# Kernel optimization log

Measured on AMD Instinct MI355X. Metric: run time of the kernel, lower is better.

## Reference

```python
import jax, jax.numpy as jnp
import numpy as np

P = 4  # polynomial kernel degree


def setup_inputs() -> dict:
    key = jax.random.key(0)
    k1, k2, k3, k4 = jax.random.split(key, 4)
    m, n, d = 16384, 8192, 64
    x_p = jax.random.normal(k1, (m, d), dtype=jnp.float32)
    X = jax.random.normal(k2, (n, d), dtype=jnp.float32)
    alpha = jax.random.uniform(k3, (n,), dtype=jnp.float32, minval=0.0, maxval=0.2)
    b = jax.random.uniform(k4, (1,), dtype=jnp.float32, minval=0.0, maxval=0.2)
    return {"x_p": x_p, "X": X, "alpha": alpha, "b": b}


def reference(x_p, X, alpha, b):
    # SVR prediction with polynomial kernel, vectorized:
    # f(x_p) = sum_i alpha_i * (1 + x_p . X_i)^P + b
    # x_p: [m, d], X: [n, d] -> K: [m, n]
    K = (1.0 + jnp.einsum('md,nd->mn', x_p, X)) ** P
    return K @ alpha + b  # [m]
```

## Files before the change

### kernel.cpp

```cpp
#include <hip/hip_runtime.h>
#include <hip/hip_bf16.h>
#include <stdint.h>


typedef __attribute__((ext_vector_type(8))) short bf16x8;
typedef __attribute__((ext_vector_type(8))) unsigned short ushort8;
typedef __attribute__((ext_vector_type(4))) float f32x4;

#define MM 16384
#define NN 8192
#define DD 64
#define NSPLIT 4
#define CHUNK 64
#define CHUNKS_PER_BLK 32
#define BM 128

__device__ __forceinline__ unsigned short f2bf(float f) {
    uint32_t u = __float_as_uint(f);
    uint32_t r = (u + 0x7FFFu + ((u >> 16) & 1u)) >> 16;
    return (unsigned short)r;
}

__device__ __forceinline__ void gll16(const void* g, void* l) {
    __builtin_amdgcn_global_load_lds(
        (const __attribute__((address_space(1))) unsigned int*)g,
        (__attribute__((address_space(3))) unsigned int*)l, 16, 0, 0);
}

__global__ void convert_kernel(const float* __restrict__ xp,
                               const float* __restrict__ X,
                               const float* __restrict__ alpha,
                               unsigned short* __restrict__ xbf,
                               unsigned short* __restrict__ Xs,
                               float* __restrict__ alpha4f) {
    const int xp4 = MM * DD / 4;
    const int xu = NN * DD / 8;
    const int tot = xp4 + xu;
    int tid0 = blockIdx.x * blockDim.x + threadIdx.x;
    if (tid0 < NN) alpha4f[tid0] = sqrtf(sqrtf(alpha[tid0]));
    int stride = gridDim.x * blockDim.x;
    for (int i = tid0; i < tot; i += stride) {
        if (i < xp4) {
            float4 v = ((const float4*)xp)[i];
            ushort4 o;
            o.x = f2bf(v.x); o.y = f2bf(v.y); o.z = f2bf(v.z); o.w = f2bf(v.w);
            *(ushort4*)(xbf + (size_t)i * 4) = o;
        } else {
            int u = i - xp4;
            int n = u >> 3;
            int slot = u & 7;
            float a4 = sqrtf(sqrtf(alpha[n]));
            float4 va = ((const float4*)X)[n * 16 + slot * 2];
            float4 vb = ((const float4*)X)[n * 16 + slot * 2 + 1];
            ushort8 o;
            o[0] = f2bf(va.x * a4); o[1] = f2bf(va.y * a4);
            o[2] = f2bf(va.z * a4); o[3] = f2bf(va.w * a4);
            o[4] = f2bf(vb.x * a4); o[5] = f2bf(vb.y * a4);
            o[6] = f2bf(vb.z * a4); o[7] = f2bf(vb.w * a4);
            size_t dst = (size_t)(n >> 6) * 4096 + (n & 63) * 64
                       + ((slot ^ (n & 7)) * 8);
            *(ushort8*)(Xs + dst) = o;
        }
    }
}

#define LOAD_B(bvar, bufp)                                            \
    {                                                                 \
        _Pragma("unroll")                                             \
        for (int nt = 0; nt < 4; ++nt) {                              \
            const int rr2 = nt * 16 + r;                              \
            const char* rowp = (bufp) + rr2 * 128;                    \
            _Pragma("unroll")                                         \
            for (int bh = 0; bh < 2; ++bh) {                          \
                const int slot = (bh * 4 + g) ^ (rr2 & 7);            \
                bvar[nt][bh] = *(const bf16x8*)(rowp + slot * 16);    \
            }                                                         \
        }                                                             \
    }

#define MFMA_SET(accv, bvar, avv)                                     \
    {                                                                 \
        _Pragma("unroll")                                             \
        for (int mt = 0; mt < 2; ++mt)                                \
            _Pragma("unroll")                                         \
            for (int nt = 0; nt < 4; ++nt)                            \
                accv[mt][nt] = (f32x4){avv[nt], avv[nt], avv[nt], avv[nt]}; \
        _Pragma("unroll")                                             \
        for (int bh = 0; bh < 2; ++bh)                                \
            _Pragma("unroll")                                         \
            for (int nt = 0; nt < 4; ++nt)                            \
                _Pragma("unroll")                                     \
                for (int mt = 0; mt < 2; ++mt)                        \
                    accv[mt][nt] = __builtin_amdgcn_mfma_f32_16x16x32_bf16( \
                        a[mt][bh], bvar[nt][bh], accv[mt][nt], 0, 0, 0);    \
    }

#define EPILOGUE(accv)                                                \
    {                                                                 \
        _Pragma("unroll")                                             \
        for (int mt = 0; mt < 2; ++mt)                                \
            _Pragma("unroll")                                         \
            for (int nt = 0; nt < 4; ++nt)                            \
                _Pragma("unroll")                                     \
                for (int i = 0; i < 4; ++i) {                         \
                    float t = accv[mt][nt][i];                        \
                    float t2 = t * t;                                 \
                    red[mt][i] = fmaf(t2, t2, red[mt][i]);            \
                }                                                     \
    }

#define STAGE(cidx)                                                   \
    {                                                                 \
        const char* gs = (const char*)Xs + (size_t)(cidx) * 8192 + tid * 16; \
        char* lb = smem + (cur ^ 1) * 8192 + w * 1024;                \
        gll16(gs, lb);                                                \
        gll16(gs + 4096, lb + 4096);                                  \
    }

__global__ __launch_bounds__(256) void svr_main(
        const unsigned short* __restrict__ xbf,
        const unsigned short* __restrict__ Xs,
        const float* __restrict__ alpha4f,
        float* __restrict__ partials) {
    __shared__ char smem[16384];
    const int tid  = threadIdx.x;
    const int lane = tid & 63;
    const int w    = tid >> 6;
    const int r    = lane & 15;
    const int g    = lane >> 4;
    const int mgroup = blockIdx.x >> 2;
    const int ns     = blockIdx.x & 3;

    bf16x8 a[2][2];
#pragma unroll
    for (int mt = 0; mt < 2; ++mt)
#pragma unroll
        for (int ks = 0; ks < 2; ++ks)
            a[mt][ks] = *(const bf16x8*)(
                xbf + (size_t)(mgroup * BM + w * 32 + mt * 16 + r) * DD
                    + ks * 32 + g * 8);

    f32x4 red[2];
#pragma unroll
    for (int mt = 0; mt < 2; ++mt) red[mt] = (f32x4){0.f, 0.f, 0.f, 0.f};

    const int chunk0 = ns * CHUNKS_PER_BLK;
    int cur = 0;

    {
        const char* gs = (const char*)Xs + (size_t)chunk0 * 8192 + tid * 16;
        char* lb = smem + w * 1024;
        gll16(gs, lb);
        gll16(gs + 4096, lb + 4096);
    }
    float av_c[4], av_n[4];
#pragma unroll
    for (int nt = 0; nt < 4; ++nt)
        av_c[nt] = alpha4f[chunk0 * CHUNK + nt * 16 + r];
    __syncthreads();

    f32x4 accE[2][4], accO[2][4];

#pragma unroll 1
    for (int p = 0; p < CHUNKS_PER_BLK / 2; ++p) {
        {
            const int cnext = chunk0 + 2 * p + 1;
            STAGE(cnext);
#pragma unroll
            for (int nt = 0; nt < 4; ++nt)
                av_n[nt] = alpha4f[cnext * CHUNK + nt * 16 + r];
        }
        {
            bf16x8 b[4][2];
            LOAD_B(b, smem + cur * 8192);
            MFMA_SET(accE, b, av_c);
        }
        if (p) EPILOGUE(accO);
        __syncthreads();
        cur ^= 1;
#pragma unroll
        for (int nt = 0; nt < 4; ++nt) av_c[nt] = av_n[nt];

        const int c1 = 2 * p + 1;
        if (c1 + 1 < CHUNKS_PER_BLK) {
            const int cnext = chunk0 + c1 + 1;
            STAGE(cnext);
#pragma unroll
            for (int nt = 0; nt < 4; ++nt)
                av_n[nt] = alpha4f[cnext * CHUNK + nt * 16 + r];
        }
        {
            bf16x8 b[4][2];
            LOAD_B(b, smem + cur * 8192);
            MFMA_SET(accO, b, av_c);
        }
        EPILOGUE(accE);
        __syncthreads();
        cur ^= 1;
        if (c1 + 1 < CHUNKS_PER_BLK) {
#pragma unroll
            for (int nt = 0; nt < 4; ++nt) av_c[nt] = av_n[nt];
        }
    }
    EPILOGUE(accO);

#pragma unroll
    for (int mt = 0; mt < 2; ++mt)
#pragma unroll
        for (int i = 0; i < 4; ++i) {
            float v = red[mt][i];
            v += __shfl_xor(v, 1);
            v += __shfl_xor(v, 2);
            v += __shfl_xor(v, 4);
            v += __shfl_xor(v, 8);
            red[mt][i] = v;
        }
    if (r == 0) {
#pragma unroll
        for (int mt = 0; mt < 2; ++mt)
#pragma unroll
            for (int i = 0; i < 4; ++i) {
                int row = mgroup * BM + w * 32 + mt * 16 + g * 4 + i;
                partials[(size_t)ns * MM + row] = red[mt][i];
            }
    }
}

__global__ void finalize_kernel(const float* __restrict__ partials,
                                const float* __restrict__ bbias,
                                float* __restrict__ out) {
    int m = blockIdx.x * blockDim.x + threadIdx.x;
    if (m < MM) {
        float s = bbias[0];
#pragma unroll
        for (int c = 0; c < NSPLIT; ++c) s += partials[(size_t)c * MM + m];
        out[m] = s;
    }
}

extern "C" void kernel_launch(void* const* d_in, const int* in_sizes, int n_in,
                              void* d_out, int out_size, void* d_ws, size_t ws_size,
                              hipStream_t stream) {
    const float* xp    = (const float*)d_in[0];
    const float* X     = (const float*)d_in[1];
    const float* alpha = (const float*)d_in[2];
    const float* b     = (const float*)d_in[3];
    float* out = (float*)d_out;

    unsigned short* xbf = (unsigned short*)d_ws;
    unsigned short* Xs  = xbf + (size_t)MM * DD;
    float* alpha4f = (float*)(Xs + (size_t)NN * DD);
    float* partials = alpha4f + NN;

    hipLaunchKernelGGL(convert_kernel, dim3(1280), dim3(256), 0, stream,
                       xp, X, alpha, xbf, Xs, alpha4f);

    hipLaunchKernelGGL(svr_main, dim3(128 * NSPLIT), dim3(256), 0, stream,
                       xbf, Xs, alpha4f, partials);

    hipLaunchKernelGGL(finalize_kernel, dim3(MM / 256), dim3(256), 0, stream,
                       partials, b, out);
}
```

Baseline: 33.98 us.

## Use four-buffer LDS ring with prefetch distance two and vmcnt-based waits

Replaces the double-buffered X staging with a four-slot LDS ring. Chunks are prefetched two steps ahead, and the two __syncthreads per pair are replaced by an explicit s_waitcnt vmcnt(12) followed by a single s_barrier per phase. The goal is to hide global-to-LDS load latency better and cut barrier overhead. LDS use doubles to 32 KB, which could reduce occupancy. The waitcnt count and the ring slot reuse must be exact to avoid races, and the final phases wrap around to stage redundant chunks.

```diff
diff --git a/kernel.cpp b/kernel.cpp
--- a/kernel.cpp
+++ b/kernel.cpp
@@ -109,12 +109,34 @@
                 }                                                     \
     }
 
-#define STAGE(cidx)                                                   \
-    {                                                                 \
-        const char* gs = (const char*)Xs + (size_t)(cidx) * 8192 + tid * 16; \
-        char* lb = smem + (cur ^ 1) * 8192 + w * 1024;                \
+#define STAGE(CLOC)                                                   \
+    {                                                                 \
+        const char* gs = (const char*)Xs                              \
+            + (size_t)(chunk0 + (CLOC)) * 8192 + tid * 16;            \
+        char* lb = smem + ((CLOC) & 3) * 8192 + w * 1024;             \
         gll16(gs, lb);                                                \
         gll16(gs + 4096, lb + 4096);                                  \
+    }
+
+#define PHASE(CLOC, ACC_THIS, ACC_PREV, DO_PREV)                      \
+    {                                                                 \
+        const int cst = ((CLOC) + 2 < CHUNKS_PER_BLK)                 \
+                          ? (CLOC) + 2 : (CLOC) + 2 - CHUNKS_PER_BLK; \
+        STAGE(cst);                                                   \
+        const int cal = ((CLOC) + 1 < CHUNKS_PER_BLK) ? (CLOC) + 1 : 0; \
+        float av_n[4];                                                \
+        _Pragma("unroll")                                             \
+        for (int nt = 0; nt < 4; ++nt)                                \
+            av_n[nt] = alpha4f[(chunk0 + cal) * CHUNK + nt * 16 + r]; \
+        asm volatile("s_waitcnt vmcnt(12)" ::: "memory");             \
+        __builtin_amdgcn_s_barrier();                                 \
+        __builtin_amdgcn_sched_barrier(0);                            \
+        bf16x8 bfr[4][2];                                             \
+        LOAD_B(bfr, smem + ((CLOC) & 3) * 8192);                      \
+        MFMA_SET(ACC_THIS, bfr, av_c);                                \
+        if (DO_PREV) EPILOGUE(ACC_PREV);                              \
+        _Pragma("unroll")                                             \
+        for (int nt = 0; nt < 4; ++nt) av_c[nt] = av_n[nt];           \
     }
 
 __global__ __launch_bounds__(256) void svr_main(
@@ -122,7 +144,7 @@
         const unsigned short* __restrict__ Xs,
         const float* __restrict__ alpha4f,
         float* __restrict__ partials) {
-    __shared__ char smem[16384];
+    __shared__ char smem[32768];
     const int tid  = threadIdx.x;
     const int lane = tid & 63;
     const int w    = tid >> 6;
@@ -145,62 +167,20 @@
     for (int mt = 0; mt < 2; ++mt) red[mt] = (f32x4){0.f, 0.f, 0.f, 0.f};
 
     const int chunk0 = ns * CHUNKS_PER_BLK;
-    int cur = 0;
-
-    {
-        const char* gs = (const char*)Xs + (size_t)chunk0 * 8192 + tid * 16;
-        char* lb = smem + w * 1024;
-        gll16(gs, lb);
-        gll16(gs + 4096, lb + 4096);
-    }
-    float av_c[4], av_n[4];
+
+    float av_c[4];
+    STAGE(0);
 #pragma unroll
     for (int nt = 0; nt < 4; ++nt)
         av_c[nt] = alpha4f[chunk0 * CHUNK + nt * 16 + r];
-    __syncthreads();
+    STAGE(1);
 
     f32x4 accE[2][4], accO[2][4];
 
 #pragma unroll 1
     for (int p = 0; p < CHUNKS_PER_BLK / 2; ++p) {
-        {
-            const int cnext = chunk0 + 2 * p + 1;
-            STAGE(cnext);
-#pragma unroll
-            for (int nt = 0; nt < 4; ++nt)
-                av_n[nt] = alpha4f[cnext * CHUNK + nt * 16 + r];
-        }
-        {
-            bf16x8 b[4][2];
-            LOAD_B(b, smem + cur * 8192);
-            MFMA_SET(accE, b, av_c);
-        }
-        if (p) EPILOGUE(accO);
-        __syncthreads();
-        cur ^= 1;
-#pragma unroll
-        for (int nt = 0; nt < 4; ++nt) av_c[nt] = av_n[nt];
-
-        const int c1 = 2 * p + 1;
-        if (c1 + 1 < CHUNKS_PER_BLK) {
-            const int cnext = chunk0 + c1 + 1;
-            STAGE(cnext);
-#pragma unroll
-            for (int nt = 0; nt < 4; ++nt)
-                av_n[nt] = alpha4f[cnext * CHUNK + nt * 16 + r];
-        }
-        {
-            bf16x8 b[4][2];
-            LOAD_B(b, smem + cur * 8192);
-            MFMA_SET(accO, b, av_c);
-        }
-        EPILOGUE(accE);
-        __syncthreads();
-        cur ^= 1;
-        if (c1 + 1 < CHUNKS_PER_BLK) {
-#pragma unroll
-            for (int nt = 0; nt < 4; ++nt) av_c[nt] = av_n[nt];
-        }
+        PHASE(2 * p,     accE, accO, (p > 0));
+        PHASE(2 * p + 1, accO, accE, true);
     }
     EPILOGUE(accO);
 
```

New measurement: 35.72 us. 5.1% more time.
